# Optimization experiments

Measured on AMD Instinct MI355X. Metric: run time of the kernel, lower is better.

The kernel has to match this reference:

```python
import jax, jax.numpy as jnp
import numpy as np

B, T, H, M = 8, 2048, 1024, 256


def setup_inputs() -> dict:
    key = jax.random.key(0)
    ks = jax.random.split(key, 8)
    hidden_states = jax.random.normal(ks[0], (B, T, H), jnp.float32)
    incoming_signal = jax.random.normal(ks[1], (B, T, H), jnp.float32)
    top_down = jax.random.normal(ks[2], (B, T, H), jnp.float32)
    basis = jax.random.normal(ks[3], (B, H, M), jnp.float32) / np.float32(np.sqrt(H))
    # coupling L = G^-1; near identity for a near-orthonormal basis
    coupling = jnp.tile(jnp.eye(M, dtype=jnp.float32), (B, 1, 1)) + 0.01 * jax.random.normal(ks[4], (B, M, M), jnp.float32)
    W_rec = jax.random.normal(ks[5], (2 * M, H), jnp.float32) / np.float32(np.sqrt(2 * M))
    tape0_re = 0.1 * jax.random.normal(ks[6], (B, M), jnp.float32)
    tape0_im = 0.1 * jax.random.normal(ks[7], (B, M), jnp.float32)
    # raw metaparams: sigmoid(gamma_raw)=0.9, softplus(beta_raw)=0.05 (init values in source)
    gamma_raw = jnp.float32(np.log(0.9 / 0.1))
    beta_raw = jnp.float32(np.log(np.expm1(0.05)))
    return dict(hidden_states=hidden_states, incoming_signal=incoming_signal, top_down=top_down,
                basis=basis, coupling=coupling, W_rec=W_rec, tape0_re=tape0_re, tape0_im=tape0_im,
                bottom_up_gain=jnp.float32(1.0), top_down_gain=jnp.float32(1.0), self_rec_gain=jnp.float32(1.0),
                gamma_raw=gamma_raw, beta_raw=beta_raw)


def reference(hidden_states, incoming_signal, top_down, basis, coupling, W_rec,
              tape0_re, tape0_im, bottom_up_gain, top_down_gain, self_rec_gain,
              gamma_raw, beta_raw):
    gamma = jax.nn.sigmoid(gamma_raw)      # transient decay
    beta = jax.nn.softplus(beta_raw)       # binding scale
    # gated combination of external + bottom-up + top-down signals
    combined = hidden_states + bottom_up_gain * incoming_signal + top_down_gain * top_down  # [B,T,H]
    # delayed self-recurrence: project real/imag tape features back into hidden space
    tape_feat = jnp.concatenate([tape0_re, tape0_im], axis=-1)          # [B,2M]
    combined = combined + self_rec_gain * (tape_feat @ W_rec)[:, None, :]
    # coupled reception (vectorized over tokens): w = E^T v ; alpha = L w
    w = jnp.einsum('btd,bdm->btm', combined, basis)                     # [B,T,M]
    alpha = jnp.einsum('btm,bmn->btn', w, coupling)                     # [B,T,M]
    # recurrent tape update (binding write + transient decay), c = alpha * s
    def step(carry, a_t):
        s_re, s_im = carry
        s_re = gamma * s_re + beta * a_t
        s_im = gamma * s_im
        return (s_re, s_im), a_t * s_re
    (_, _), c_re = jax.lax.scan(step, (tape0_re, tape0_im), jnp.swapaxes(alpha, 0, 1))
    c_re = jnp.swapaxes(c_re, 0, 1)                                     # [B,T,M]
    # readout through the basis
    y = jnp.einsum('btm,bdm->btd', c_re, basis)                         # [B,T,H]
    return y
```

## Files before the change

kernel.cpp:

```cpp
#include <hip/hip_runtime.h>
#include <hip/hip_bf16.h>

#define B_  8
#define T_  2048
#define H_  1024
#define M_  256

typedef __bf16 bf16x8 __attribute__((ext_vector_type(8)));
typedef float  f32x4  __attribute__((ext_vector_type(4)));
typedef unsigned short us4 __attribute__((ext_vector_type(4)));
typedef unsigned short us8 __attribute__((ext_vector_type(8)));

__device__ inline unsigned short f2bf(float f) {
    unsigned int u = __builtin_bit_cast(unsigned int, f);
    return (unsigned short)((u + 0x7FFFu + ((u >> 16) & 1u)) >> 16);
}
__device__ inline float bf2f(unsigned short u) {
    unsigned int x = ((unsigned int)u) << 16;
    return __builtin_bit_cast(float, x);
}

__global__ void k_prep(const float* __restrict__ basis, const float* __restrict__ cpl,
                       const float* __restrict__ W, const float* __restrict__ re,
                       const float* __restrict__ im, const float* __restrict__ g_srg,
                       unsigned short* __restrict__ basisB, unsigned short* __restrict__ cplT,
                       float* __restrict__ bias)
{
    int blk = blockIdx.x;
    int tid = threadIdx.x;
    if (blk < 1024) {
        size_t i = ((size_t)blk * 256 + tid) * 8;
        float4 a = *(const float4*)&basis[i];
        float4 b = *(const float4*)&basis[i + 4];
        us8 o = { f2bf(a.x), f2bf(a.y), f2bf(a.z), f2bf(a.w),
                  f2bf(b.x), f2bf(b.y), f2bf(b.z), f2bf(b.w) };
        *(us8*)&basisB[i] = o;
    } else if (blk < 1152) {
        int idx = blk - 1024;
        int x = idx & 3, y = (idx >> 2) & 3, b = idx >> 4;
        int r0 = x * 64, c0 = y * 64;
        __shared__ float t[64][65];
        #pragma unroll
        for (int i = 0; i < 4; ++i) {
            int u = tid + i * 256;
            int r = u >> 4, c4 = (u & 15) * 4;
            float4 v = *(const float4*)&cpl[((size_t)(b * M_ + r0 + r)) * M_ + c0 + c4];
            t[r][c4] = v.x; t[r][c4 + 1] = v.y; t[r][c4 + 2] = v.z; t[r][c4 + 3] = v.w;
        }
        __syncthreads();
        #pragma unroll
        for (int i = 0; i < 4; ++i) {
            int u = tid + i * 256;
            int m = u >> 4, r4 = (u & 15) * 4;
            us4 o = { f2bf(t[r4][m]), f2bf(t[r4 + 1][m]), f2bf(t[r4 + 2][m]), f2bf(t[r4 + 3][m]) };
            *(us4*)&cplT[((size_t)(b * M_ + c0 + m)) * M_ + r0 + r4] = o;
        }
    } else {
        int idx = blk - 1152;
        int b = idx & 7, h0 = (idx >> 3) * 64;
        int lane = tid & 63, w = tid >> 6;
        int h = h0 + lane;
        float acc = 0.f;
        #pragma unroll 4
        for (int m = w * 64; m < w * 64 + 64; ++m) {
            float rv = re[b * M_ + m], iv = im[b * M_ + m];
            acc += rv * W[(size_t)m * H_ + h] + iv * W[(size_t)(M_ + m) * H_ + h];
        }
        __shared__ float sh[4][64];
        sh[w][lane] = acc;
        __syncthreads();
        if (w == 0)
            bias[b * H_ + h] = g_srg[0] * (sh[0][lane] + sh[1][lane] + sh[2][lane] + sh[3][lane]);
    }
}

__global__ __launch_bounds__(256) void k_b2(const unsigned short* __restrict__ cplT,
                                            const unsigned short* __restrict__ basisB,
                                            unsigned short* __restrict__ b2T)
{
    const int b = blockIdx.z;
    const int n0 = blockIdx.x * 64;
    const int h0 = blockIdx.y * 128;
    const int tid = threadIdx.x;
    const int lane = tid & 63, w = tid >> 6;

    __shared__ __align__(16) unsigned short As[64][72];
    __shared__ __align__(16) unsigned short Bs[128][72];

    const unsigned short* Ab = cplT + (size_t)(b * M_ + n0) * M_;
    const unsigned short* Bb = basisB + (size_t)(b * H_ + h0) * M_;

    f32x4 acc[4][2];
    #pragma unroll
    for (int i = 0; i < 4; ++i) { acc[i][0] = (f32x4){0,0,0,0}; acc[i][1] = (f32x4){0,0,0,0}; }

    const int rsel = lane & 15;
    const int kgrp = (lane >> 4) * 8;

    for (int k0 = 0; k0 < M_; k0 += 64) {
        #pragma unroll
        for (int i = 0; i < 2; ++i) {
            int u = tid + i * 256;
            int r = u >> 3, c8 = (u & 7) * 8;
            *(us8*)&As[r][c8] = *(const us8*)&Ab[(size_t)r * M_ + k0 + c8];
        }
        #pragma unroll
        for (int i = 0; i < 4; ++i) {
            int u = tid + i * 256;
            int r = u >> 3, c8 = (u & 7) * 8;
            *(us8*)&Bs[r][c8] = *(const us8*)&Bb[(size_t)r * M_ + k0 + c8];
        }
        __syncthreads();
        #pragma unroll
        for (int kk = 0; kk < 2; ++kk) {
            const int kb = kk * 32 + kgrp;
            bf16x8 af[4], bfr[2];
            #pragma unroll
            for (int mi = 0; mi < 4; ++mi) af[mi] = *(const bf16x8*)&As[mi * 16 + rsel][kb];
            #pragma unroll
            for (int ni = 0; ni < 2; ++ni) bfr[ni] = *(const bf16x8*)&Bs[w * 32 + ni * 16 + rsel][kb];
            #pragma unroll
            for (int mi = 0; mi < 4; ++mi)
                #pragma unroll
                for (int ni = 0; ni < 2; ++ni)
                    acc[mi][ni] = __builtin_amdgcn_mfma_f32_16x16x32_bf16(af[mi], bfr[ni], acc[mi][ni], 0, 0, 0);
        }
        __syncthreads();
    }

    unsigned short* ob = b2T + (size_t)(b * M_ + n0) * H_ + h0;
    const int rbase = (lane >> 4) * 4;
    #pragma unroll
    for (int mi = 0; mi < 4; ++mi)
        #pragma unroll
        for (int ni = 0; ni < 2; ++ni)
            #pragma unroll
            for (int r = 0; r < 4; ++r)
                ob[(size_t)(mi * 16 + rbase + r) * H_ + w * 32 + ni * 16 + rsel] = f2bf(acc[mi][ni][r]);
}

__global__ __launch_bounds__(512) void k_alpha(
    const float* __restrict__ hs, const float* __restrict__ inc, const float* __restrict__ tdn,
    const unsigned short* __restrict__ b2T, const float* __restrict__ bias,
    const float* __restrict__ g_bu, const float* __restrict__ g_td,
    unsigned short* __restrict__ alpha16)
{
    const int b = blockIdx.y;
    const int t0 = blockIdx.x * 32;
    const int tid = threadIdx.x;
    const int lane = tid & 63, w = tid >> 6;
    const float bug = g_bu[0], tdg = g_td[0];

    __shared__ __align__(16) unsigned short As[32][72];
    __shared__ __align__(16) unsigned short Bs[256][72];

    const float* hsb = hs  + (size_t)(b * T_ + t0) * H_;
    const float* inb = inc + (size_t)(b * T_ + t0) * H_;
    const float* tdb = tdn + (size_t)(b * T_ + t0) * H_;
    const float* bib = bias + (size_t)b * H_;
    const unsigned short* Bb = b2T + (size_t)b * M_ * H_;

    const int ar  = tid >> 4;
    const int ac4 = (tid & 15) * 4;
    const int br0 = tid >> 3;
    const int bc8 = (tid & 7) * 8;

    f32x4 acc[2][2];
    acc[0][0] = (f32x4){0,0,0,0}; acc[0][1] = (f32x4){0,0,0,0};
    acc[1][0] = (f32x4){0,0,0,0}; acc[1][1] = (f32x4){0,0,0,0};

    const int rsel = lane & 15;
    const int kgrp = (lane >> 4) * 8;

    float4 pa, pe, pd, pbv;
    us8 pB0, pB1, pB2, pB3;

    #define LOAD_TILE(K0) do {                                                  \
        size_t g = (size_t)ar * H_ + (K0) + ac4;                                \
        pa  = *(const float4*)(hsb + g);                                        \
        pe  = *(const float4*)(inb + g);                                        \
        pd  = *(const float4*)(tdb + g);                                        \
        pbv = *(const float4*)(bib + (K0) + ac4);                               \
        pB0 = *(const us8*)&Bb[(size_t)(br0      ) * H_ + (K0) + bc8];          \
        pB1 = *(const us8*)&Bb[(size_t)(br0 +  64) * H_ + (K0) + bc8];          \
        pB2 = *(const us8*)&Bb[(size_t)(br0 + 128) * H_ + (K0) + bc8];          \
        pB3 = *(const us8*)&Bb[(size_t)(br0 + 192) * H_ + (K0) + bc8];          \
    } while (0)

    #define STORE_TILE() do {                                                   \
        us4 o = { f2bf(pa.x + bug * pe.x + tdg * pd.x + pbv.x),                 \
                  f2bf(pa.y + bug * pe.y + tdg * pd.y + pbv.y),                 \
                  f2bf(pa.z + bug * pe.z + tdg * pd.z + pbv.z),                 \
                  f2bf(pa.w + bug * pe.w + tdg * pd.w + pbv.w) };               \
        *(us4*)&As[ar][ac4] = o;                                                \
        *(us8*)&Bs[br0      ][bc8] = pB0;                                       \
        *(us8*)&Bs[br0 +  64][bc8] = pB1;                                       \
        *(us8*)&Bs[br0 + 128][bc8] = pB2;                                       \
        *(us8*)&Bs[br0 + 192][bc8] = pB3;                                       \
    } while (0)

    #define COMPUTE_TILE() do {                                                 \
        _Pragma("unroll")                                                       \
        for (int kk = 0; kk < 2; ++kk) {                                        \
            const int kb = kk * 32 + kgrp;                                      \
            bf16x8 af0 = *(const bf16x8*)&As[rsel][kb];                         \
            bf16x8 af1 = *(const bf16x8*)&As[16 + rsel][kb];                    \
            bf16x8 bf0 = *(const bf16x8*)&Bs[w * 32 + rsel][kb];                \
            bf16x8 bf1 = *(const bf16x8*)&Bs[w * 32 + 16 + rsel][kb];           \
            acc[0][0] = __builtin_amdgcn_mfma_f32_16x16x32_bf16(af0, bf0, acc[0][0], 0, 0, 0); \
            acc[0][1] = __builtin_amdgcn_mfma_f32_16x16x32_bf16(af0, bf1, acc[0][1], 0, 0, 0); \
            acc[1][0] = __builtin_amdgcn_mfma_f32_16x16x32_bf16(af1, bf0, acc[1][0], 0, 0, 0); \
            acc[1][1] = __builtin_amdgcn_mfma_f32_16x16x32_bf16(af1, bf1, acc[1][1], 0, 0, 0); \
        }                                                                       \
    } while (0)

    LOAD_TILE(0);
    STORE_TILE();
    __syncthreads();
    for (int k0 = 64; k0 < H_; k0 += 64) {
        LOAD_TILE(k0);
        COMPUTE_TILE();
        __syncthreads();
        STORE_TILE();
        __syncthreads();
    }
    COMPUTE_TILE();

    #undef LOAD_TILE
    #undef STORE_TILE
    #undef COMPUTE_TILE

    unsigned short* ab = alpha16 + (size_t)(b * T_ + t0) * M_;
    const int rbase = (lane >> 4) * 4;
    #pragma unroll
    for (int mi = 0; mi < 2; ++mi)
        #pragma unroll
        for (int ni = 0; ni < 2; ++ni)
            #pragma unroll
            for (int r = 0; r < 4; ++r)
                ab[(size_t)(mi * 16 + rbase + r) * M_ + w * 32 + ni * 16 + rsel] = f2bf(acc[mi][ni][r]);
}

__global__ void k_scan(const unsigned short* __restrict__ alpha16, const float* __restrict__ tape_re,
                       const float* __restrict__ g_gr, const float* __restrict__ g_br,
                       unsigned short* __restrict__ cbuf)
{
    int b = blockIdx.y, chunk = blockIdx.x;
    int m = threadIdx.x;
    float graw = g_gr[0], braw = g_br[0];
    float gamma = 1.f / (1.f + __expf(-graw));
    float beta  = log1pf(__expf(braw));
    int t0 = chunk * 64;
    int th = (t0 >= 96) ? (t0 - 96) : 0;
    float s = tape_re[b * M_ + m];
    if (th > 0) s *= __powf(gamma, (float)th);
    const unsigned short* ab = alpha16 + (size_t)b * T_ * M_ + m;
    unsigned short* cb = cbuf + (size_t)b * T_ * M_ + m;
    for (int t = th; t < t0 + 64; ++t) {
        float a = bf2f(ab[(size_t)t * M_]);
        s = gamma * s + beta * a;
        if (t >= t0) cb[(size_t)t * M_] = f2bf(a * s);
    }
}

__global__ __launch_bounds__(256) void k_y(const unsigned short* __restrict__ cbuf,
                                           const unsigned short* __restrict__ basisB,
                                           float* __restrict__ out)
{
    const int b = blockIdx.z;
    const int t0 = blockIdx.x * 128;
    const int h0 = blockIdx.y * 128;
    const int tid = threadIdx.x;
    const int lane = tid & 63, w = tid >> 6;
    const int wm = w >> 1, wn = w & 1;

    __shared__ __align__(16) unsigned short As[128][72];
    __shared__ __align__(16) unsigned short Bs[128][72];

    const unsigned short* cb = cbuf + (size_t)(b * T_ + t0) * M_;
    const unsigned short* bb = basisB + (size_t)(b * H_ + h0) * M_;

    f32x4 acc[4][4];
    #pragma unroll
    for (int i = 0; i < 4; ++i)
        #pragma unroll
        for (int j = 0; j < 4; ++j)
            acc[i][j] = (f32x4){0.f, 0.f, 0.f, 0.f};

    const int rsel = lane & 15;
    const int kgrp = (lane >> 4) * 8;

    for (int k0 = 0; k0 < M_; k0 += 64) {
        #pragma unroll
        for (int i = 0; i < 4; ++i) {
            int u = tid + i * 256;
            int r = u >> 3, c8 = (u & 7) * 8;
            *(us8*)&As[r][c8] = *(const us8*)&cb[(size_t)r * M_ + k0 + c8];
        }
        #pragma unroll
        for (int i = 0; i < 4; ++i) {
            int u = tid + i * 256;
            int r = u >> 3, c8 = (u & 7) * 8;
            *(us8*)&Bs[r][c8] = *(const us8*)&bb[(size_t)r * M_ + k0 + c8];
        }
        __syncthreads();
        #pragma unroll
        for (int kk = 0; kk < 2; ++kk) {
            const int kb = kk * 32 + kgrp;
            bf16x8 af[4], bfr[4];
            #pragma unroll
            for (int mi = 0; mi < 4; ++mi) af[mi] = *(const bf16x8*)&As[wm * 64 + mi * 16 + rsel][kb];
            #pragma unroll
            for (int ni = 0; ni < 4; ++ni) bfr[ni] = *(const bf16x8*)&Bs[wn * 64 + ni * 16 + rsel][kb];
            #pragma unroll
            for (int mi = 0; mi < 4; ++mi)
                #pragma unroll
                for (int ni = 0; ni < 4; ++ni)
                    acc[mi][ni] = __builtin_amdgcn_mfma_f32_16x16x32_bf16(af[mi], bfr[ni], acc[mi][ni], 0, 0, 0);
        }
        __syncthreads();
    }

    float* ob = out + (size_t)(b * T_ + t0) * H_ + h0;
    const int rbase = (lane >> 4) * 4;
    #pragma unroll
    for (int mi = 0; mi < 4; ++mi)
        #pragma unroll
        for (int ni = 0; ni < 4; ++ni)
            #pragma unroll
            for (int r = 0; r < 4; ++r)
                ob[(size_t)(wm * 64 + mi * 16 + rbase + r) * H_ + wn * 64 + ni * 16 + rsel] = acc[mi][ni][r];
}

extern "C" void kernel_launch(void* const* d_in, const int* in_sizes, int n_in,
                              void* d_out, int out_size, void* d_ws, size_t ws_size,
                              hipStream_t stream)
{
    const float* hs   = (const float*)d_in[0];
    const float* inc  = (const float*)d_in[1];
    const float* tdn  = (const float*)d_in[2];
    const float* basis= (const float*)d_in[3];
    const float* cpl  = (const float*)d_in[4];
    const float* W    = (const float*)d_in[5];
    const float* t_re = (const float*)d_in[6];
    const float* t_im = (const float*)d_in[7];
    const float* g_bu = (const float*)d_in[8];
    const float* g_td = (const float*)d_in[9];
    const float* g_sr = (const float*)d_in[10];
    const float* g_gr = (const float*)d_in[11];
    const float* g_br = (const float*)d_in[12];
    float* out = (float*)d_out;

    char* ws = (char*)d_ws;
    float*          bias   = (float*)(ws);
    unsigned short* basisB = (unsigned short*)(ws + (1u << 16));
    unsigned short* cplT   = (unsigned short*)(ws + (1u << 16) + (4u << 20));
    unsigned short* b2T    = (unsigned short*)(ws + (1u << 16) + (5u << 20));
    unsigned short* alpha16= (unsigned short*)(ws + (1u << 16) + (9u << 20));
    unsigned short* cbuf   = (unsigned short*)(ws + (1u << 16) + (17u << 20));

    k_prep <<<dim3(1280),                   dim3(256),  0, stream>>>(basis, cpl, W, t_re, t_im, g_sr, basisB, cplT, bias);
    k_b2   <<<dim3(M_ / 64, H_ / 128, B_),  dim3(256),  0, stream>>>(cplT, basisB, b2T);
    k_alpha<<<dim3(T_ / 32, B_),            dim3(512),  0, stream>>>(hs, inc, tdn, b2T, bias, g_bu, g_td, alpha16);
    k_scan <<<dim3(T_ / 64, B_),            dim3(256),  0, stream>>>(alpha16, t_re, g_gr, g_br, cbuf);
    k_y    <<<dim3(T_ / 128, H_ / 128, B_), dim3(256),  0, stream>>>(cbuf, basisB, out);
}
```

Baseline: 149.5 us.

## Rewrite alpha and readout GEMMs to load MFMA fragments directly from global memory

```diff
diff --git a/kernel.cpp b/kernel.cpp
--- a/kernel.cpp
+++ b/kernel.cpp
@@ -139,106 +139,80 @@
                 ob[(size_t)(mi * 16 + rbase + r) * H_ + w * 32 + ni * 16 + rsel] = f2bf(acc[mi][ni][r]);
 }
 
-__global__ __launch_bounds__(512) void k_alpha(
+__global__ __launch_bounds__(256, 1) void k_alpha(
     const float* __restrict__ hs, const float* __restrict__ inc, const float* __restrict__ tdn,
     const unsigned short* __restrict__ b2T, const float* __restrict__ bias,
     const float* __restrict__ g_bu, const float* __restrict__ g_td,
     unsigned short* __restrict__ alpha16)
 {
-    const int b = blockIdx.y;
-    const int t0 = blockIdx.x * 32;
+    const int flat = blockIdx.x;
+    const int b = flat & 7;
+    const int t0 = (flat >> 3) * 64;
     const int tid = threadIdx.x;
-    const int lane = tid & 63, w = tid >> 6;
+    const int lane = tid & 63, wid = tid >> 6;
+    const int wt = (wid & 1) * 32;
+    const int mh = (wid >> 1) * 128;
+    const int rsel = lane & 15;
+    const int kgo = (lane >> 4) * 8;
     const float bug = g_bu[0], tdg = g_td[0];
 
-    __shared__ __align__(16) unsigned short As[32][72];
-    __shared__ __align__(16) unsigned short Bs[256][72];
-
-    const float* hsb = hs  + (size_t)(b * T_ + t0) * H_;
-    const float* inb = inc + (size_t)(b * T_ + t0) * H_;
-    const float* tdb = tdn + (size_t)(b * T_ + t0) * H_;
-    const float* bib = bias + (size_t)b * H_;
-    const unsigned short* Bb = b2T + (size_t)b * M_ * H_;
-
-    const int ar  = tid >> 4;
-    const int ac4 = (tid & 15) * 4;
-    const int br0 = tid >> 3;
-    const int bc8 = (tid & 7) * 8;
-
-    f32x4 acc[2][2];
-    acc[0][0] = (f32x4){0,0,0,0}; acc[0][1] = (f32x4){0,0,0,0};
-    acc[1][0] = (f32x4){0,0,0,0}; acc[1][1] = (f32x4){0,0,0,0};
-
-    const int rsel = lane & 15;
-    const int kgrp = (lane >> 4) * 8;
-
-    float4 pa, pe, pd, pbv;
-    us8 pB0, pB1, pB2, pB3;
-
-    #define LOAD_TILE(K0) do {                                                  \
-        size_t g = (size_t)ar * H_ + (K0) + ac4;                                \
-        pa  = *(const float4*)(hsb + g);                                        \
-        pe  = *(const float4*)(inb + g);                                        \
-        pd  = *(const float4*)(tdb + g);                                        \
-        pbv = *(const float4*)(bib + (K0) + ac4);                               \
-        pB0 = *(const us8*)&Bb[(size_t)(br0      ) * H_ + (K0) + bc8];          \
-        pB1 = *(const us8*)&Bb[(size_t)(br0 +  64) * H_ + (K0) + bc8];          \
-        pB2 = *(const us8*)&Bb[(size_t)(br0 + 128) * H_ + (K0) + bc8];          \
-        pB3 = *(const us8*)&Bb[(size_t)(br0 + 192) * H_ + (K0) + bc8];          \
-    } while (0)
-
-    #define STORE_TILE() do {                                                   \
-        us4 o = { f2bf(pa.x + bug * pe.x + tdg * pd.x + pbv.x),                 \
-                  f2bf(pa.y + bug * pe.y + tdg * pd.y + pbv.y),                 \
-                  f2bf(pa.z + bug * pe.z + tdg * pd.z + pbv.z),                 \
-                  f2bf(pa.w + bug * pe.w + tdg * pd.w + pbv.w) };               \
-        *(us4*)&As[ar][ac4] = o;                                                \
-        *(us8*)&Bs[br0      ][bc8] = pB0;                                       \
-        *(us8*)&Bs[br0 +  64][bc8] = pB1;                                       \
-        *(us8*)&Bs[br0 + 128][bc8] = pB2;                                       \
-        *(us8*)&Bs[br0 + 192][bc8] = pB3;                                       \
-    } while (0)
-
-    #define COMPUTE_TILE() do {                                                 \
-        _Pragma("unroll")                                                       \
-        for (int kk = 0; kk < 2; ++kk) {                                        \
-            const int kb = kk * 32 + kgrp;                                      \
-            bf16x8 af0 = *(const bf16x8*)&As[rsel][kb];                         \
-            bf16x8 af1 = *(const bf16x8*)&As[16 + rsel][kb];                    \
-            bf16x8 bf0 = *(const bf16x8*)&Bs[w * 32 + rsel][kb];                \
-            bf16x8 bf1 = *(const bf16x8*)&Bs[w * 32 + 16 + rsel][kb];           \
-            acc[0][0] = __builtin_amdgcn_mfma_f32_16x16x32_bf16(af0, bf0, acc[0][0], 0, 0, 0); \
-            acc[0][1] = __builtin_amdgcn_mfma_f32_16x16x32_bf16(af0, bf1, acc[0][1], 0, 0, 0); \
-            acc[1][0] = __builtin_amdgcn_mfma_f32_16x16x32_bf16(af1, bf0, acc[1][0], 0, 0, 0); \
-            acc[1][1] = __builtin_amdgcn_mfma_f32_16x16x32_bf16(af1, bf1, acc[1][1], 0, 0, 0); \
-        }                                                                       \
-    } while (0)
-
-    LOAD_TILE(0);
-    STORE_TILE();
-    __syncthreads();
-    for (int k0 = 64; k0 < H_; k0 += 64) {
-        LOAD_TILE(k0);
-        COMPUTE_TILE();
-        __syncthreads();
-        STORE_TILE();
-        __syncthreads();
-    }
-    COMPUTE_TILE();
-
-    #undef LOAD_TILE
-    #undef STORE_TILE
-    #undef COMPUTE_TILE
-
-    unsigned short* ab = alpha16 + (size_t)(b * T_ + t0) * M_;
+    const size_t rb0 = ((size_t)(b * T_) + t0 + wt + rsel) * H_ + kgo;
+    const size_t rb1 = rb0 + (size_t)16 * H_;
+    const float* hs0 = hs + rb0;  const float* hs1 = hs + rb1;
+    const float* in0 = inc + rb0; const float* in1 = inc + rb1;
+    const float* td0 = tdn + rb0; const float* td1 = tdn + rb1;
+    const float* bib = bias + b * H_ + kgo;
+    const unsigned short* Bb = b2T + ((size_t)(b * M_) + mh + rsel) * H_ + kgo;
+
+    f32x4 acc[2][8];
+    #pragma unroll
+    for (int i = 0; i < 2; ++i)
+        #pragma unroll
+        for (int j = 0; j < 8; ++j)
+            acc[i][j] = (f32x4){0.f, 0.f, 0.f, 0.f};
+
+    #pragma unroll 2
+    for (int kb = 0; kb < H_; kb += 32) {
+        f32x4 bi0 = *(const f32x4*)(bib + kb);
+        f32x4 bi1 = *(const f32x4*)(bib + kb + 4);
+        f32x4 a00 = *(const f32x4*)(hs0 + kb), a01 = *(const f32x4*)(hs0 + kb + 4);
+        f32x4 e00 = *(const f32x4*)(in0 + kb), e01 = *(const f32x4*)(in0 + kb + 4);
+        f32x4 d00 = *(const f32x4*)(td0 + kb), d01 = *(const f32x4*)(td0 + kb + 4);
+        f32x4 a10 = *(const f32x4*)(hs1 + kb), a11 = *(const f32x4*)(hs1 + kb + 4);
+        f32x4 e10 = *(const f32x4*)(in1 + kb), e11 = *(const f32x4*)(in1 + kb + 4);
+        f32x4 d10 = *(const f32x4*)(td1 + kb), d11 = *(const f32x4*)(td1 + kb + 4);
+
+        f32x4 c00 = a00 + bug * e00 + tdg * d00 + bi0;
+        f32x4 c01 = a01 + bug * e01 + tdg * d01 + bi1;
+        f32x4 c10 = a10 + bug * e10 + tdg * d10 + bi0;
+        f32x4 c11 = a11 + bug * e11 + tdg * d11 + bi1;
+
+        bf16x8 af0, af1;
+        #pragma unroll
+        for (int j = 0; j < 4; ++j) {
+            af0[j]     = (__bf16)c00[j];
+            af0[j + 4] = (__bf16)c01[j];
+            af1[j]     = (__bf16)c10[j];
+            af1[j + 4] = (__bf16)c11[j];
+        }
+
+        #pragma unroll
+        for (int ni = 0; ni < 8; ++ni) {
+            bf16x8 bv = *(const bf16x8*)(Bb + (size_t)ni * (16 * H_) + kb);
+            acc[0][ni] = __builtin_amdgcn_mfma_f32_16x16x32_bf16(af0, bv, acc[0][ni], 0, 0, 0);
+            acc[1][ni] = __builtin_amdgcn_mfma_f32_16x16x32_bf16(af1, bv, acc[1][ni], 0, 0, 0);
+        }
+    }
+
+    unsigned short* ab = alpha16 + ((size_t)(b * T_) + t0 + wt) * M_ + mh;
     const int rbase = (lane >> 4) * 4;
     #pragma unroll
-    for (int mi = 0; mi < 2; ++mi)
-        #pragma unroll
-        for (int ni = 0; ni < 2; ++ni)
+    for (int ti = 0; ti < 2; ++ti)
+        #pragma unroll
+        for (int ni = 0; ni < 8; ++ni)
             #pragma unroll
             for (int r = 0; r < 4; ++r)
-                ab[(size_t)(mi * 16 + rbase + r) * M_ + w * 32 + ni * 16 + rsel] = f2bf(acc[mi][ni][r]);
+                ab[(size_t)(ti * 16 + rbase + r) * M_ + ni * 16 + rsel] = f2bf(acc[ti][ni][r]);
 }
 
 __global__ void k_scan(const unsigned short* __restrict__ alpha16, const float* __restrict__ tape_re,
@@ -263,73 +237,46 @@
     }
 }
 
-__global__ __launch_bounds__(256) void k_y(const unsigned short* __restrict__ cbuf,
-                                           const unsigned short* __restrict__ basisB,
-                                           float* __restrict__ out)
-{
-    const int b = blockIdx.z;
-    const int t0 = blockIdx.x * 128;
-    const int h0 = blockIdx.y * 128;
+__global__ __launch_bounds__(256, 4) void k_y(const unsigned short* __restrict__ cbuf,
+                                              const unsigned short* __restrict__ basisB,
+                                              float* __restrict__ out)
+{
+    const int flat = blockIdx.x;
+    const int b = flat & 7;
+    const int q = flat >> 3;
+    const int t0 = (q & 63) * 32;
+    const int h0 = (q >> 6) * 256;
     const int tid = threadIdx.x;
-    const int lane = tid & 63, w = tid >> 6;
-    const int wm = w >> 1, wn = w & 1;
-
-    __shared__ __align__(16) unsigned short As[128][72];
-    __shared__ __align__(16) unsigned short Bs[128][72];
-
-    const unsigned short* cb = cbuf + (size_t)(b * T_ + t0) * M_;
-    const unsigned short* bb = basisB + (size_t)(b * H_ + h0) * M_;
-
-    f32x4 acc[4][4];
-    #pragma unroll
-    for (int i = 0; i < 4; ++i)
-        #pragma unroll
-        for (int j = 0; j < 4; ++j)
-            acc[i][j] = (f32x4){0.f, 0.f, 0.f, 0.f};
-
+    const int lane = tid & 63, wid = tid >> 6;
+    const int wt = (wid & 1) * 16;
+    const int hh = (wid >> 1) * 128;
     const int rsel = lane & 15;
-    const int kgrp = (lane >> 4) * 8;
-
-    for (int k0 = 0; k0 < M_; k0 += 64) {
-        #pragma unroll
-        for (int i = 0; i < 4; ++i) {
-            int u = tid + i * 256;
-            int r = u >> 3, c8 = (u & 7) * 8;
-            *(us8*)&As[r][c8] = *(const us8*)&cb[(size_t)r * M_ + k0 + c8];
-        }
-        #pragma unroll
-        for (int i = 0; i < 4; ++i) {
-            int u = tid + i * 256;
-            int r = u >> 3, c8 = (u & 7) * 8;
-            *(us8*)&Bs[r][c8] = *(const us8*)&bb[(size_t)r * M_ + k0 + c8];
-        }
-        __syncthreads();
-        #pragma unroll
-        for (int kk = 0; kk < 2; ++kk) {
-            const int kb = kk * 32 + kgrp;
-            bf16x8 af[4], bfr[4];
-            #pragma unroll
-            for (int mi = 0; mi < 4; ++mi) af[mi] = *(const bf16x8*)&As[wm * 64 + mi * 16 + rsel][kb];
-            #pragma unroll
-            for (int ni = 0; ni < 4; ++ni) bfr[ni] = *(const bf16x8*)&Bs[wn * 64 + ni * 16 + rsel][kb];
-            #pragma unroll
-            for (int mi = 0; mi < 4; ++mi)
-                #pragma unroll
-                for (int ni = 0; ni < 4; ++ni)
-                    acc[mi][ni] = __builtin_amdgcn_mfma_f32_16x16x32_bf16(af[mi], bfr[ni], acc[mi][ni], 0, 0, 0);
-        }
-        __syncthreads();
-    }
-
-    float* ob = out + (size_t)(b * T_ + t0) * H_ + h0;
+    const int kgo = (lane >> 4) * 8;
+
+    const unsigned short* At = cbuf + ((size_t)(b * T_) + t0 + wt + rsel) * M_ + kgo;
+    const unsigned short* Bh = basisB + ((size_t)(b * H_) + h0 + hh + rsel) * M_ + kgo;
+
+    f32x4 acc[8];
+    #pragma unroll
+    for (int i = 0; i < 8; ++i) acc[i] = (f32x4){0.f, 0.f, 0.f, 0.f};
+
+    #pragma unroll
+    for (int kb = 0; kb < M_; kb += 32) {
+        bf16x8 af = *(const bf16x8*)(At + kb);
+        #pragma unroll
+        for (int ni = 0; ni < 8; ++ni) {
+            bf16x8 bv = *(const bf16x8*)(Bh + (size_t)ni * (16 * M_) + kb);
+            acc[ni] = __builtin_amdgcn_mfma_f32_16x16x32_bf16(af, bv, acc[ni], 0, 0, 0);
+        }
+    }
+
+    float* ob = out + ((size_t)(b * T_) + t0 + wt) * H_ + h0 + hh;
     const int rbase = (lane >> 4) * 4;
     #pragma unroll
-    for (int mi = 0; mi < 4; ++mi)
-        #pragma unroll
-        for (int ni = 0; ni < 4; ++ni)
-            #pragma unroll
-            for (int r = 0; r < 4; ++r)
-                ob[(size_t)(wm * 64 + mi * 16 + rbase + r) * H_ + wn * 64 + ni * 16 + rsel] = acc[mi][ni][r];
+    for (int ni = 0; ni < 8; ++ni)
+        #pragma unroll
+        for (int r = 0; r < 4; ++r)
+            ob[(size_t)(rbase + r) * H_ + ni * 16 + rsel] = acc[ni][r];
 }
 
 extern "C" void kernel_launch(void* const* d_in, const int* in_sizes, int n_in,
@@ -359,9 +306,9 @@
     unsigned short* alpha16= (unsigned short*)(ws + (1u << 16) + (9u << 20));
     unsigned short* cbuf   = (unsigned short*)(ws + (1u << 16) + (17u << 20));
 
-    k_prep <<<dim3(1280),                   dim3(256),  0, stream>>>(basis, cpl, W, t_re, t_im, g_sr, basisB, cplT, bias);
-    k_b2   <<<dim3(M_ / 64, H_ / 128, B_),  dim3(256),  0, stream>>>(cplT, basisB, b2T);
-    k_alpha<<<dim3(T_ / 32, B_),            dim3(512),  0, stream>>>(hs, inc, tdn, b2T, bias, g_bu, g_td, alpha16);
-    k_scan <<<dim3(T_ / 64, B_),            dim3(256),  0, stream>>>(alpha16, t_re, g_gr, g_br, cbuf);
-    k_y    <<<dim3(T_ / 128, H_ / 128, B_), dim3(256),  0, stream>>>(cbuf, basisB, out);
-}
+    k_prep <<<dim3(1280),                  dim3(256), 0, stream>>>(basis, cpl, W, t_re, t_im, g_sr, basisB, cplT, bias);
+    k_b2   <<<dim3(M_ / 64, H_ / 128, B_), dim3(256), 0, stream>>>(cplT, basisB, b2T);
+    k_alpha<<<dim3(256),                   dim3(256), 0, stream>>>(hs, inc, tdn, b2T, bias, g_bu, g_td, alpha16);
+    k_scan <<<dim3(T_ / 64, B_),           dim3(256), 0, stream>>>(alpha16, t_re, g_gr, g_br, cbuf);
+    k_y    <<<dim3(2048),                  dim3(256), 0, stream>>>(cbuf, basisB, out);
+}
```

Result: slower. 248.7 us (+66.3%).
